# Kernel tuning notes

Measured on AMD Instinct MI355X. Metric: run time of the kernel, lower is better.

Reference implementation:

```python
import jax, jax.numpy as jnp
import numpy as np

B, C, H, W = 8, 64, 128, 128
O, KS, STRIDE, PAD = 64, 3, 1, 1
K = KS * KS


def setup_inputs() -> dict:
    key = jax.random.key(0)
    k1, k2, k3 = jax.random.split(key, 3)
    x = jax.random.normal(k1, (B, C, H, W), dtype=jnp.float32)
    offset = jax.random.normal(k2, (B, 2 * K, H, W), dtype=jnp.float32)
    weight = jax.random.normal(k3, (O, C, KS, KS), dtype=jnp.float32)
    bias = jnp.zeros((O,), dtype=jnp.float32)
    return {"x": x, "offset": offset, "weight": weight, "bias": bias}


def _deform_conv(x, offset, weight, bias, ks=KS, stride=STRIDE, pad=PAD):
    Bx, Cx, Hx, Wx = x.shape
    Kk = ks * ks
    Ho = (Hx + 2 * pad - ks) // stride + 1
    Wo = (Wx + 2 * pad - ks) // stride + 1
    x_pad = jnp.pad(x, ((0, 0), (0, 0), (pad, pad), (pad, pad)))
    Hp, Wp = Hx + 2 * pad, Wx + 2 * pad
    # base grid (top-left tap, padded coords) -- matches torch code exactly
    ys = jnp.arange(Ho, dtype=x.dtype) * stride
    xs = jnp.arange(Wo, dtype=x.dtype) * stride
    off = offset.reshape(Bx, Kk, 2, Ho, Wo).astype(x.dtype)
    gx = off[:, :, 0] + xs[None, None, None, :]   # [B,K,Ho,Wo]
    gy = off[:, :, 1] + ys[None, None, :, None]
    # bilinear sample with zeros padding (grid_sample align_corners=True round-trips
    # normalization exactly, so we sample at (gy,gx) directly)
    x0 = jnp.floor(gx); y0 = jnp.floor(gy)
    wx1 = gx - x0; wx0 = 1.0 - wx1
    wy1 = gy - y0; wy0 = 1.0 - wy1
    x_flat = x_pad.reshape(Bx, Cx, Hp * Wp)

    def gather(yi, xi, w):
        valid = (xi >= 0) & (xi <= Wp - 1) & (yi >= 0) & (yi <= Hp - 1)
        xi_c = jnp.clip(xi, 0, Wp - 1).astype(jnp.int32)
        yi_c = jnp.clip(yi, 0, Hp - 1).astype(jnp.int32)
        idx = (yi_c * Wp + xi_c).reshape(Bx, -1)           # [B, K*Ho*Wo]
        g = jnp.take_along_axis(x_flat, idx[:, None, :], axis=2)  # [B,C,K*Ho*Wo]
        wv = (w * valid.astype(x.dtype)).reshape(Bx, 1, -1)
        return g * wv

    acc = (gather(y0, x0, wy0 * wx0)
           + gather(y0, x0 + 1.0, wy0 * wx1)
           + gather(y0 + 1.0, x0, wy1 * wx0)
           + gather(y0 + 1.0, x0 + 1.0, wy1 * wx1))
    # channel layout after torch.cat over k: index = k*C + c (k-major)
    sampled = acc.reshape(Bx, Cx, Kk, Ho, Wo).transpose(0, 2, 1, 3, 4)
    sampled = sampled.reshape(Bx, Kk * Cx, Ho, Wo)
    # torch flattens weight as (c, kh, kw) -> index = c*K + k; faithful mismatch
    w_flat = weight.reshape(weight.shape[0], -1).astype(sampled.dtype)  # [O, C*K]
    out = jnp.einsum('oi,bihw->bohw', w_flat, sampled)
    return out + bias[None, :, None, None]


def reference(x, offset, weight, bias):
    return _deform_conv(x, offset, weight, bias)
```

## Files before the change

### kernel.cpp

```cpp
#include <hip/hip_runtime.h>
#include <hip/hip_bf16.h>

#define BB 8
#define CC 64
#define OO 64
#define HH 128
#define WWI 128
#define HWSZ (HH * WWI)
#define KK 9
#define II (KK * CC)

#define PXW 16
#define PYH 16
#define WNX 24
#define WNY 24
#define WROWS (WNX * WNY)

typedef __attribute__((ext_vector_type(8))) _Float16 half8;
typedef __attribute__((ext_vector_type(2))) _Float16 h2;
typedef __attribute__((ext_vector_type(4))) float f32x4;
typedef __attribute__((ext_vector_type(4))) unsigned int uint4v;

__device__ __forceinline__ int iclamp(int v, int lo, int hi) {
    return v < lo ? lo : (v > hi ? hi : v);
}
__device__ __forceinline__ unsigned short f2h(float f) {
    union { _Float16 h; unsigned short s; } v;
    v.h = (_Float16)f;
    return v.s;
}
__device__ __forceinline__ h2 u2h(unsigned u) {
    union { unsigned u; h2 h; } v;
    v.u = u;
    return v.h;
}

__global__ __launch_bounds__(256) void prep_xt(const float* __restrict__ x,
                                               unsigned short* __restrict__ xt) {
    __shared__ float tile[64][65];
    const int blk = blockIdx.x;
    const int b = blk & 7;
    const int p0 = (blk >> 3) * 64;
    const int t = threadIdx.x;
    const int a = t >> 6;
    const int q = t & 63;
    const float* xb = x + (size_t)b * CC * HWSZ + p0;
#pragma unroll
    for (int r = 0; r < 16; ++r) {
        int c = r * 4 + a;
        tile[c][q] = xb[(size_t)c * HWSZ + q];
    }
    __syncthreads();
    unsigned short* xo = xt + ((size_t)b * HWSZ + p0) * CC;
#pragma unroll
    for (int r = 0; r < 16; ++r) {
        int pl = r * 4 + a;
        xo[(size_t)pl * CC + q] = f2h(tile[q][pl]);
    }
}

__global__ void prep_waf(const float* __restrict__ w, unsigned short* __restrict__ waf) {
    int tid = blockIdx.x * 256 + threadIdx.x;
    if (tid < 72 * 512) {
        int slab = tid >> 9;
        int r = tid & 511;
        int l = r >> 3, j = r & 7;
        int m = slab & 3;
        int kc = (slab >> 2) & 1;
        int k = slab >> 3;
        int o = m * 16 + (l & 15);
        int i = k * 64 + kc * 32 + (l >> 4) * 8 + j;
        waf[tid] = f2h(w[(size_t)o * II + i]);
    }
}

__global__ __launch_bounds__(512, 3) void deform_mfma7(
        const unsigned short* __restrict__ xt,
        const float* __restrict__ off,
        const unsigned short* __restrict__ waf,
        const float* __restrict__ bias,
        float* __restrict__ out) {
    extern __shared__ unsigned short win[];

    const int blk = blockIdx.x;
    const int b = blk & 7;
    const int pidx = blk >> 3;
    const int y0 = (pidx >> 3) * PYH;
    const int x0 = (pidx & 7) * PXW;
    const int xleft = x0 - 4, ytop = y0 - 4;

    const int t = threadIdx.x;
    const int wave = t >> 6;
    const int lane = t & 63;
    const int fm = lane & 15;
    const int hi = lane >> 4;
    const int c0s = hi * 8;
    const int c1s = 32 + hi * 8;

    const unsigned short* xtb = xt + (size_t)b * HWSZ * CC;
    const float* offpx = off + (size_t)b * 2 * KK * HWSZ
                             + (size_t)(y0 + wave * 2) * WWI + x0 + fm;

    float oxb[2][2], oyb[2][2];
#pragma unroll
    for (int nt = 0; nt < 2; ++nt) {
        oxb[0][nt] = offpx[(size_t)0 * HWSZ + nt * WWI];
        oyb[0][nt] = offpx[(size_t)1 * HWSZ + nt * WWI];
    }

    {
        const int tch = t & 7;
        const int rb = t >> 3;
#pragma unroll
        for (int sw = 0; sw < 9; ++sw) {
            const int r = sw * 64 + rb;
            const int wy = r / WNX, wx = r - wy * WNX;
            const int cy = ytop + wy, cx = xleft + wx;
            if (((unsigned)cy < (unsigned)HH) && ((unsigned)cx < (unsigned)WWI)) {
                const uint4v v = *(const uint4v*)(xtb + (size_t)(cy * WWI + cx) * CC + tch * 8);
                *(uint4v*)&win[r * CC + ((tch ^ (r & 7)) << 3)] = v;
            }
        }
    }
    __syncthreads();

    f32x4 acc[2][4];
#pragma unroll
    for (int nt = 0; nt < 2; ++nt)
#pragma unroll
        for (int m = 0; m < 4; ++m) acc[nt][m] = (f32x4)(0.0f);

#pragma unroll
    for (int k = 0; k < KK; ++k) {
        const int cur = k & 1, nxt = cur ^ 1;
        if (k + 1 < KK) {
#pragma unroll
            for (int nt = 0; nt < 2; ++nt) {
                oxb[nxt][nt] = offpx[(size_t)(2 * k + 2) * HWSZ + nt * WWI];
                oyb[nxt][nt] = offpx[(size_t)(2 * k + 3) * HWSZ + nt * WWI];
            }
        }
        const unsigned short* wk = waf + (size_t)k * 8 * 512 + lane * 8;
        half8 af[8];
#pragma unroll
        for (int q = 0; q < 8; ++q) af[q] = *(const half8*)(wk + (size_t)q * 512);

#pragma unroll
        for (int nt = 0; nt < 2; ++nt) {
            const float gx = oxb[cur][nt] + (float)(x0 + fm);
            const float gy = oyb[cur][nt] + (float)(y0 + wave * 2 + nt);
            const float fxf = floorf(gx), fyf = floorf(gy);
            const float fx = gx - fxf, fy = gy - fyf;
            const int ux0 = (int)fxf - 1, ux1 = (int)fxf;
            const int uy0 = (int)fyf - 1, uy1 = (int)fyf;
            const float vx0 = ((unsigned)ux0 < (unsigned)WWI) ? 1.0f : 0.0f;
            const float vx1 = ((unsigned)ux1 < (unsigned)WWI) ? 1.0f : 0.0f;
            const float vy0 = ((unsigned)uy0 < (unsigned)HH) ? 1.0f : 0.0f;
            const float vy1 = ((unsigned)uy1 < (unsigned)HH) ? 1.0f : 0.0f;
            const float w00 = (1.0f - fy) * (1.0f - fx) * vy0 * vx0;
            const float w01 = (1.0f - fy) * fx          * vy0 * vx1;
            const float w10 = fy          * (1.0f - fx) * vy1 * vx0;
            const float w11 = fy          * fx          * vy1 * vx1;
            const int cx0 = iclamp(ux0, 0, WWI - 1), cx1 = iclamp(ux1, 0, WWI - 1);
            const int cy0 = iclamp(uy0, 0, HH - 1),  cy1 = iclamp(uy1, 0, HH - 1);

            const bool inw = (cx0 >= xleft) & (cx1 <= xleft + WNX - 1)
                           & (cy0 >= ytop) & (cy1 <= ytop + WNY - 1);
            const int wx0 = iclamp(cx0 - xleft, 0, WNX - 1);
            const int wx1 = iclamp(cx1 - xleft, 0, WNX - 1);
            const int wy0 = iclamp(cy0 - ytop, 0, WNY - 1);
            const int wy1 = iclamp(cy1 - ytop, 0, WNY - 1);
            const int r00 = wy0 * WNX + wx0, r01 = wy0 * WNX + wx1;
            const int r10 = wy1 * WNX + wx0, r11 = wy1 * WNX + wx1;

#define LDSRD(r, kc) (*(const uint4v*)&win[(r) * CC + ((((hi) + ((kc) << 2)) ^ ((r) & 7)) << 3)])
            uint4v A0 = LDSRD(r00, 0), A1 = LDSRD(r00, 1);
            uint4v B0 = LDSRD(r01, 0), B1 = LDSRD(r01, 1);
            uint4v C0 = LDSRD(r10, 0), C1 = LDSRD(r10, 1);
            uint4v D0 = LDSRD(r11, 0), D1 = LDSRD(r11, 1);
#undef LDSRD
            if (!inw) {
                const unsigned short* g00 = xtb + (size_t)(cy0 * WWI + cx0) * CC;
                const unsigned short* g01 = xtb + (size_t)(cy0 * WWI + cx1) * CC;
                const unsigned short* g10 = xtb + (size_t)(cy1 * WWI + cx0) * CC;
                const unsigned short* g11 = xtb + (size_t)(cy1 * WWI + cx1) * CC;
                A0 = *(const uint4v*)(g00 + c0s);  A1 = *(const uint4v*)(g00 + c1s);
                B0 = *(const uint4v*)(g01 + c0s);  B1 = *(const uint4v*)(g01 + c1s);
                C0 = *(const uint4v*)(g10 + c0s);  C1 = *(const uint4v*)(g10 + c1s);
                D0 = *(const uint4v*)(g11 + c0s);  D1 = *(const uint4v*)(g11 + c1s);
            }

            const _Float16 hw00 = (_Float16)w00, hw01 = (_Float16)w01;
            const _Float16 hw10 = (_Float16)w10, hw11 = (_Float16)w11;
            const h2 w00v = {hw00, hw00}, w01v = {hw01, hw01};
            const h2 w10v = {hw10, hw10}, w11v = {hw11, hw11};
            half8 bf0, bf1;
            h2* rp0 = (h2*)&bf0;
            h2* rp1 = (h2*)&bf1;
#pragma unroll
            for (int i = 0; i < 4; ++i) {
                h2 r0 = u2h(A0[i]) * w00v;
                r0 += u2h(B0[i]) * w01v;
                r0 += u2h(C0[i]) * w10v;
                r0 += u2h(D0[i]) * w11v;
                rp0[i] = r0;
                h2 r1 = u2h(A1[i]) * w00v;
                r1 += u2h(B1[i]) * w01v;
                r1 += u2h(C1[i]) * w10v;
                r1 += u2h(D1[i]) * w11v;
                rp1[i] = r1;
            }
#pragma unroll
            for (int m = 0; m < 4; ++m)
                acc[nt][m] = __builtin_amdgcn_mfma_f32_16x16x32_f16(af[m], bf0, acc[nt][m], 0, 0, 0);
#pragma unroll
            for (int m = 0; m < 4; ++m)
                acc[nt][m] = __builtin_amdgcn_mfma_f32_16x16x32_f16(af[4 + m], bf1, acc[nt][m], 0, 0, 0);
        }
    }

#pragma unroll
    for (int nt = 0; nt < 2; ++nt) {
        float* outb = out + (size_t)b * OO * HWSZ
                          + (size_t)(y0 + wave * 2 + nt) * WWI + x0 + fm;
#pragma unroll
        for (int m = 0; m < 4; ++m) {
            const int ob = m * 16 + hi * 4;
            const float4 bs = *(const float4*)(bias + ob);
#pragma unroll
            for (int j = 0; j < 4; ++j) {
                outb[(size_t)(ob + j) * HWSZ] = acc[nt][m][j] + ((const float*)&bs)[j];
            }
        }
    }
}

__global__ __launch_bounds__(256) void deform_conv_fallback(
        const float* __restrict__ x, const float* __restrict__ off,
        const float* __restrict__ wmat, const float* __restrict__ bias,
        float* __restrict__ out) {
    const int b = blockIdx.y;
    const int p = blockIdx.x * 256 + threadIdx.x;
    const int wo = p & (WWI - 1);
    const int ho = p >> 7;
    const float* xb = x + (size_t)b * CC * HWSZ;
    const float* offb = off + (size_t)b * 2 * KK * HWSZ + p;
    float acc[OO];
#pragma unroll
    for (int o = 0; o < OO; ++o) acc[o] = 0.0f;
#pragma unroll 1
    for (int k = 0; k < KK; ++k) {
        const float gx = offb[(size_t)(2 * k + 0) * HWSZ] + (float)wo;
        const float gy = offb[(size_t)(2 * k + 1) * HWSZ] + (float)ho;
        const float fxf = floorf(gx), fyf = floorf(gy);
        const float fx = gx - fxf, fy = gy - fyf;
        const int ux0 = (int)fxf - 1, ux1 = (int)fxf;
        const int uy0 = (int)fyf - 1, uy1 = (int)fyf;
        const float vx0 = ((unsigned)ux0 < (unsigned)WWI) ? 1.0f : 0.0f;
        const float vx1 = ((unsigned)ux1 < (unsigned)WWI) ? 1.0f : 0.0f;
        const float vy0 = ((unsigned)uy0 < (unsigned)HH) ? 1.0f : 0.0f;
        const float vy1 = ((unsigned)uy1 < (unsigned)HH) ? 1.0f : 0.0f;
        const float w00 = (1.0f - fy) * (1.0f - fx) * vy0 * vx0;
        const float w01 = (1.0f - fy) * fx * vy0 * vx1;
        const float w10 = fy * (1.0f - fx) * vy1 * vx0;
        const float w11 = fy * fx * vy1 * vx1;
        const int cx0 = iclamp(ux0, 0, WWI - 1), cx1 = iclamp(ux1, 0, WWI - 1);
        const int cy0 = iclamp(uy0, 0, HH - 1), cy1 = iclamp(uy1, 0, HH - 1);
        const int i00 = cy0 * WWI + cx0, i01 = cy0 * WWI + cx1;
        const int i10 = cy1 * WWI + cx0, i11 = cy1 * WWI + cx1;
#pragma unroll 4
        for (int c = 0; c < CC; ++c) {
            const float* xc = xb + (size_t)c * HWSZ;
            const float v = w00 * xc[i00] + w01 * xc[i01] + w10 * xc[i10] + w11 * xc[i11];
            const float* wrow = wmat + (size_t)(k * CC + c);
#pragma unroll
            for (int o = 0; o < OO; ++o) acc[o] = fmaf(wrow[(size_t)o * II], v, acc[o]);
        }
    }
    float* outb = out + (size_t)b * OO * HWSZ + p;
#pragma unroll
    for (int o = 0; o < OO; ++o) outb[(size_t)o * HWSZ] = acc[o] + bias[o];
}

extern "C" void kernel_launch(void* const* d_in, const int* in_sizes, int n_in,
                              void* d_out, int out_size, void* d_ws, size_t ws_size,
                              hipStream_t stream) {
    const float* x    = (const float*)d_in[0];
    const float* off  = (const float*)d_in[1];
    const float* w    = (const float*)d_in[2];
    const float* bias = (const float*)d_in[3];
    float* out = (float*)d_out;

    const size_t xt_bytes  = (size_t)BB * HWSZ * CC * sizeof(unsigned short);
    const size_t waf_bytes = (size_t)72 * 512 * sizeof(unsigned short);

    if (ws_size >= xt_bytes + waf_bytes) {
        unsigned short* xt  = (unsigned short*)d_ws;
        unsigned short* wfp = (unsigned short*)((char*)d_ws + xt_bytes);
        prep_xt<<<dim3((HWSZ / 64) * BB), 256, 0, stream>>>(x, xt);
        prep_waf<<<(72 * 512 + 255) / 256, 256, 0, stream>>>(w, wfp);
        deform_mfma7<<<dim3(BB * (HH / PYH) * (WWI / PXW)), dim3(512),
                       WROWS * CC * sizeof(unsigned short), stream>>>(
            xt, off, wfp, bias, out);
    } else {
        deform_conv_fallback<<<dim3(HWSZ / 256, BB), 256, 0, stream>>>(x, off, w, bias, out);
    }
}
```

Measured before the change: 50.91 us.

## Software-pipeline LDS gathers one tap ahead and deepen offset prefetch

Restructures the tap loop into a manually unrolled ISSUE/PROC pipeline. LDS reads for the next (tap, row) unit are issued before the current unit's bilinear blend and MFMAs, so LDS latency overlaps with compute. Offset prefetch goes from one tap ahead to two, and weight fragments are double-buffered. The extra registers this needs force the launch-bounds occupancy hint down from 3 to 2 blocks per CU, so latency hiding from having more waves resident is traded for latency hiding inside each wave.

Measured after the change: 46.54 us. -8.6%, faster.

```diff
diff --git a/kernel.cpp b/kernel.cpp
--- a/kernel.cpp
+++ b/kernel.cpp
@@ -74,7 +74,7 @@
     }
 }
 
-__global__ __launch_bounds__(512, 3) void deform_mfma7(
+__global__ __launch_bounds__(512, 2) void deform_mfma9(
         const unsigned short* __restrict__ xt,
         const float* __restrict__ off,
         const unsigned short* __restrict__ waf,
@@ -101,11 +101,14 @@
     const float* offpx = off + (size_t)b * 2 * KK * HWSZ
                              + (size_t)(y0 + wave * 2) * WWI + x0 + fm;
 
-    float oxb[2][2], oyb[2][2];
-#pragma unroll
-    for (int nt = 0; nt < 2; ++nt) {
-        oxb[0][nt] = offpx[(size_t)0 * HWSZ + nt * WWI];
-        oyb[0][nt] = offpx[(size_t)1 * HWSZ + nt * WWI];
+    float ox[3][2], oy[3][2];
+#pragma unroll
+    for (int k = 0; k < 2; ++k) {
+#pragma unroll
+        for (int nt = 0; nt < 2; ++nt) {
+            ox[k][nt] = offpx[(size_t)(2 * k + 0) * HWSZ + nt * WWI];
+            oy[k][nt] = offpx[(size_t)(2 * k + 1) * HWSZ + nt * WWI];
+        }
     }
 
     {
@@ -130,94 +133,136 @@
 #pragma unroll
         for (int m = 0; m < 4; ++m) acc[nt][m] = (f32x4)(0.0f);
 
-#pragma unroll
-    for (int k = 0; k < KK; ++k) {
-        const int cur = k & 1, nxt = cur ^ 1;
-        if (k + 1 < KK) {
-#pragma unroll
-            for (int nt = 0; nt < 2; ++nt) {
-                oxb[nxt][nt] = offpx[(size_t)(2 * k + 2) * HWSZ + nt * WWI];
-                oyb[nxt][nt] = offpx[(size_t)(2 * k + 3) * HWSZ + nt * WWI];
-            }
-        }
-        const unsigned short* wk = waf + (size_t)k * 8 * 512 + lane * 8;
-        half8 af[8];
-#pragma unroll
-        for (int q = 0; q < 8; ++q) af[q] = *(const half8*)(wk + (size_t)q * 512);
-
-#pragma unroll
-        for (int nt = 0; nt < 2; ++nt) {
-            const float gx = oxb[cur][nt] + (float)(x0 + fm);
-            const float gy = oyb[cur][nt] + (float)(y0 + wave * 2 + nt);
-            const float fxf = floorf(gx), fyf = floorf(gy);
-            const float fx = gx - fxf, fy = gy - fyf;
-            const int ux0 = (int)fxf - 1, ux1 = (int)fxf;
-            const int uy0 = (int)fyf - 1, uy1 = (int)fyf;
-            const float vx0 = ((unsigned)ux0 < (unsigned)WWI) ? 1.0f : 0.0f;
-            const float vx1 = ((unsigned)ux1 < (unsigned)WWI) ? 1.0f : 0.0f;
-            const float vy0 = ((unsigned)uy0 < (unsigned)HH) ? 1.0f : 0.0f;
-            const float vy1 = ((unsigned)uy1 < (unsigned)HH) ? 1.0f : 0.0f;
-            const float w00 = (1.0f - fy) * (1.0f - fx) * vy0 * vx0;
-            const float w01 = (1.0f - fy) * fx          * vy0 * vx1;
-            const float w10 = fy          * (1.0f - fx) * vy1 * vx0;
-            const float w11 = fy          * fx          * vy1 * vx1;
-            const int cx0 = iclamp(ux0, 0, WWI - 1), cx1 = iclamp(ux1, 0, WWI - 1);
-            const int cy0 = iclamp(uy0, 0, HH - 1),  cy1 = iclamp(uy1, 0, HH - 1);
-
-            const bool inw = (cx0 >= xleft) & (cx1 <= xleft + WNX - 1)
-                           & (cy0 >= ytop) & (cy1 <= ytop + WNY - 1);
-            const int wx0 = iclamp(cx0 - xleft, 0, WNX - 1);
-            const int wx1 = iclamp(cx1 - xleft, 0, WNX - 1);
-            const int wy0 = iclamp(cy0 - ytop, 0, WNY - 1);
-            const int wy1 = iclamp(cy1 - ytop, 0, WNY - 1);
-            const int r00 = wy0 * WNX + wx0, r01 = wy0 * WNX + wx1;
-            const int r10 = wy1 * WNX + wx0, r11 = wy1 * WNX + wx1;
+    uint4v cb[2][8];
+    float  cw[2][4];
+    bool   inwf[2];
+    int    gidx[2][4];
+    half8  afb[2][8];
 
 #define LDSRD(r, kc) (*(const uint4v*)&win[(r) * CC + ((((hi) + ((kc) << 2)) ^ ((r) & 7)) << 3)])
-            uint4v A0 = LDSRD(r00, 0), A1 = LDSRD(r00, 1);
-            uint4v B0 = LDSRD(r01, 0), B1 = LDSRD(r01, 1);
-            uint4v C0 = LDSRD(r10, 0), C1 = LDSRD(r10, 1);
-            uint4v D0 = LDSRD(r11, 0), D1 = LDSRD(r11, 1);
+
+#define ISSUE(u) do {                                                           \
+        if ((((u) & 1) == 0) && (((u) >> 1) + 2 < KK)) {                        \
+            _Pragma("unroll")                                                   \
+            for (int nt = 0; nt < 2; ++nt) {                                    \
+                ox[(((u) >> 1) + 2) % 3][nt] =                                  \
+                    offpx[(size_t)(2 * (((u) >> 1) + 2) + 0) * HWSZ + nt * WWI];\
+                oy[(((u) >> 1) + 2) % 3][nt] =                                  \
+                    offpx[(size_t)(2 * (((u) >> 1) + 2) + 1) * HWSZ + nt * WWI];\
+            }                                                                   \
+        }                                                                       \
+        if (((u) & 1) == 0) {                                                   \
+            const unsigned short* wk = waf + (size_t)((u) >> 1) * 8 * 512 + lane * 8; \
+            _Pragma("unroll")                                                   \
+            for (int q = 0; q < 8; ++q)                                         \
+                afb[((u) >> 1) & 1][q] = *(const half8*)(wk + (size_t)q * 512); \
+        }                                                                       \
+        const float gx = ox[((u) >> 1) % 3][(u) & 1] + (float)(x0 + fm);        \
+        const float gy = oy[((u) >> 1) % 3][(u) & 1] + (float)(y0 + wave * 2 + ((u) & 1)); \
+        const float fxf = floorf(gx), fyf = floorf(gy);                         \
+        const float fx = gx - fxf, fy = gy - fyf;                               \
+        const int ux0 = (int)fxf - 1, ux1 = (int)fxf;                           \
+        const int uy0 = (int)fyf - 1, uy1 = (int)fyf;                           \
+        const float vx0 = ((unsigned)ux0 < (unsigned)WWI) ? 1.0f : 0.0f;        \
+        const float vx1 = ((unsigned)ux1 < (unsigned)WWI) ? 1.0f : 0.0f;        \
+        const float vy0 = ((unsigned)uy0 < (unsigned)HH) ? 1.0f : 0.0f;         \
+        const float vy1 = ((unsigned)uy1 < (unsigned)HH) ? 1.0f : 0.0f;         \
+        cw[(u) & 1][0] = (1.0f - fy) * (1.0f - fx) * vy0 * vx0;                 \
+        cw[(u) & 1][1] = (1.0f - fy) * fx          * vy0 * vx1;                 \
+        cw[(u) & 1][2] = fy          * (1.0f - fx) * vy1 * vx0;                 \
+        cw[(u) & 1][3] = fy          * fx          * vy1 * vx1;                 \
+        const int cx0 = iclamp(ux0, 0, WWI - 1), cx1 = iclamp(ux1, 0, WWI - 1); \
+        const int cy0 = iclamp(uy0, 0, HH - 1),  cy1 = iclamp(uy1, 0, HH - 1);  \
+        inwf[(u) & 1] = (cx0 >= xleft) & (cx1 <= xleft + WNX - 1)               \
+                      & (cy0 >= ytop) & (cy1 <= ytop + WNY - 1);                \
+        gidx[(u) & 1][0] = cy0 * WWI + cx0;  gidx[(u) & 1][1] = cy0 * WWI + cx1;\
+        gidx[(u) & 1][2] = cy1 * WWI + cx0;  gidx[(u) & 1][3] = cy1 * WWI + cx1;\
+        const int wx0 = iclamp(cx0 - xleft, 0, WNX - 1);                        \
+        const int wx1 = iclamp(cx1 - xleft, 0, WNX - 1);                        \
+        const int wy0 = iclamp(cy0 - ytop, 0, WNY - 1);                         \
+        const int wy1 = iclamp(cy1 - ytop, 0, WNY - 1);                         \
+        const int r00 = wy0 * WNX + wx0, r01 = wy0 * WNX + wx1;                 \
+        const int r10 = wy1 * WNX + wx0, r11 = wy1 * WNX + wx1;                 \
+        cb[(u) & 1][0] = LDSRD(r00, 0);  cb[(u) & 1][1] = LDSRD(r00, 1);        \
+        cb[(u) & 1][2] = LDSRD(r01, 0);  cb[(u) & 1][3] = LDSRD(r01, 1);        \
+        cb[(u) & 1][4] = LDSRD(r10, 0);  cb[(u) & 1][5] = LDSRD(r10, 1);        \
+        cb[(u) & 1][6] = LDSRD(r11, 0);  cb[(u) & 1][7] = LDSRD(r11, 1);        \
+    } while (0)
+
+#define PROC(u) do {                                                            \
+        asm volatile("" : "+v"(cb[(u) & 1][0]), "+v"(cb[(u) & 1][1]),           \
+                          "+v"(cb[(u) & 1][2]), "+v"(cb[(u) & 1][3]),           \
+                          "+v"(cb[(u) & 1][4]), "+v"(cb[(u) & 1][5]),           \
+                          "+v"(cb[(u) & 1][6]), "+v"(cb[(u) & 1][7]));          \
+        uint4v A0 = cb[(u) & 1][0], A1 = cb[(u) & 1][1];                        \
+        uint4v B0 = cb[(u) & 1][2], B1 = cb[(u) & 1][3];                        \
+        uint4v C0 = cb[(u) & 1][4], C1 = cb[(u) & 1][5];                        \
+        uint4v D0 = cb[(u) & 1][6], D1 = cb[(u) & 1][7];                        \
+        if (!inwf[(u) & 1]) {                                                   \
+            const unsigned short* g00 = xtb + (size_t)gidx[(u) & 1][0] * CC;    \
+            const unsigned short* g01 = xtb + (size_t)gidx[(u) & 1][1] * CC;    \
+            const unsigned short* g10 = xtb + (size_t)gidx[(u) & 1][2] * CC;    \
+            const unsigned short* g11 = xtb + (size_t)gidx[(u) & 1][3] * CC;    \
+            A0 = *(const uint4v*)(g00 + c0s);  A1 = *(const uint4v*)(g00 + c1s);\
+            B0 = *(const uint4v*)(g01 + c0s);  B1 = *(const uint4v*)(g01 + c1s);\
+            C0 = *(const uint4v*)(g10 + c0s);  C1 = *(const uint4v*)(g10 + c1s);\
+            D0 = *(const uint4v*)(g11 + c0s);  D1 = *(const uint4v*)(g11 + c1s);\
+        }                                                                       \
+        const _Float16 hw00 = (_Float16)cw[(u) & 1][0];                         \
+        const _Float16 hw01 = (_Float16)cw[(u) & 1][1];                         \
+        const _Float16 hw10 = (_Float16)cw[(u) & 1][2];                         \
+        const _Float16 hw11 = (_Float16)cw[(u) & 1][3];                         \
+        const h2 w00v = {hw00, hw00}, w01v = {hw01, hw01};                      \
+        const h2 w10v = {hw10, hw10}, w11v = {hw11, hw11};                      \
+        half8 bf0, bf1;                                                         \
+        h2* rp0 = (h2*)&bf0;                                                    \
+        h2* rp1 = (h2*)&bf1;                                                    \
+        _Pragma("unroll")                                                       \
+        for (int i = 0; i < 4; ++i) {                                           \
+            h2 r0 = u2h(A0[i]) * w00v;                                          \
+            r0 += u2h(B0[i]) * w01v;                                            \
+            r0 += u2h(C0[i]) * w10v;                                            \
+            r0 += u2h(D0[i]) * w11v;                                            \
+            rp0[i] = r0;                                                        \
+            h2 r1 = u2h(A1[i]) * w00v;                                          \
+            r1 += u2h(B1[i]) * w01v;                                            \
+            r1 += u2h(C1[i]) * w10v;                                            \
+            r1 += u2h(D1[i]) * w11v;                                            \
+            rp1[i] = r1;                                                        \
+        }                                                                       \
+        _Pragma("unroll")                                                       \
+        for (int m = 0; m < 4; ++m)                                             \
+            acc[(u) & 1][m] = __builtin_amdgcn_mfma_f32_16x16x32_f16(           \
+                afb[((u) >> 1) & 1][m], bf0, acc[(u) & 1][m], 0, 0, 0);         \
+        _Pragma("unroll")                                                       \
+        for (int m = 0; m < 4; ++m)                                             \
+            acc[(u) & 1][m] = __builtin_amdgcn_mfma_f32_16x16x32_f16(           \
+                afb[((u) >> 1) & 1][4 + m], bf1, acc[(u) & 1][m], 0, 0, 0);     \
+    } while (0)
+
+    ISSUE(0);  ISSUE(1);
+    PROC(0);   ISSUE(2);
+    PROC(1);   ISSUE(3);
+    PROC(2);   ISSUE(4);
+    PROC(3);   ISSUE(5);
+    PROC(4);   ISSUE(6);
+    PROC(5);   ISSUE(7);
+    PROC(6);   ISSUE(8);
+    PROC(7);   ISSUE(9);
+    PROC(8);   ISSUE(10);
+    PROC(9);   ISSUE(11);
+    PROC(10);  ISSUE(12);
+    PROC(11);  ISSUE(13);
+    PROC(12);  ISSUE(14);
+    PROC(13);  ISSUE(15);
+    PROC(14);  ISSUE(16);
+    PROC(15);  ISSUE(17);
+    PROC(16);
+    PROC(17);
+
+#undef ISSUE
+#undef PROC
 #undef LDSRD
-            if (!inw) {
-                const unsigned short* g00 = xtb + (size_t)(cy0 * WWI + cx0) * CC;
-                const unsigned short* g01 = xtb + (size_t)(cy0 * WWI + cx1) * CC;
-                const unsigned short* g10 = xtb + (size_t)(cy1 * WWI + cx0) * CC;
-                const unsigned short* g11 = xtb + (size_t)(cy1 * WWI + cx1) * CC;
-                A0 = *(const uint4v*)(g00 + c0s);  A1 = *(const uint4v*)(g00 + c1s);
-                B0 = *(const uint4v*)(g01 + c0s);  B1 = *(const uint4v*)(g01 + c1s);
-                C0 = *(const uint4v*)(g10 + c0s);  C1 = *(const uint4v*)(g10 + c1s);
-                D0 = *(const uint4v*)(g11 + c0s);  D1 = *(const uint4v*)(g11 + c1s);
-            }
-
-            const _Float16 hw00 = (_Float16)w00, hw01 = (_Float16)w01;
-            const _Float16 hw10 = (_Float16)w10, hw11 = (_Float16)w11;
-            const h2 w00v = {hw00, hw00}, w01v = {hw01, hw01};
-            const h2 w10v = {hw10, hw10}, w11v = {hw11, hw11};
-            half8 bf0, bf1;
-            h2* rp0 = (h2*)&bf0;
-            h2* rp1 = (h2*)&bf1;
-#pragma unroll
-            for (int i = 0; i < 4; ++i) {
-                h2 r0 = u2h(A0[i]) * w00v;
-                r0 += u2h(B0[i]) * w01v;
-                r0 += u2h(C0[i]) * w10v;
-                r0 += u2h(D0[i]) * w11v;
-                rp0[i] = r0;
-                h2 r1 = u2h(A1[i]) * w00v;
-                r1 += u2h(B1[i]) * w01v;
-                r1 += u2h(C1[i]) * w10v;
-                r1 += u2h(D1[i]) * w11v;
-                rp1[i] = r1;
-            }
-#pragma unroll
-            for (int m = 0; m < 4; ++m)
-                acc[nt][m] = __builtin_amdgcn_mfma_f32_16x16x32_f16(af[m], bf0, acc[nt][m], 0, 0, 0);
-#pragma unroll
-            for (int m = 0; m < 4; ++m)
-                acc[nt][m] = __builtin_amdgcn_mfma_f32_16x16x32_f16(af[4 + m], bf1, acc[nt][m], 0, 0, 0);
-        }
-    }
 
 #pragma unroll
     for (int nt = 0; nt < 2; ++nt) {
@@ -299,7 +344,7 @@
         unsigned short* wfp = (unsigned short*)((char*)d_ws + xt_bytes);
         prep_xt<<<dim3((HWSZ / 64) * BB), 256, 0, stream>>>(x, xt);
         prep_waf<<<(72 * 512 + 255) / 256, 256, 0, stream>>>(w, wfp);
-        deform_mfma7<<<dim3(BB * (HH / PYH) * (WWI / PXW)), dim3(512),
+        deform_mfma9<<<dim3(BB * (HH / PYH) * (WWI / PXW)), dim3(512),
                        WROWS * CC * sizeof(unsigned short), stream>>>(
             xt, off, wfp, bias, out);
     } else {
```
